# Kernel optimization log

Hardware: AMD Instinct MI355X
Metric: run time of the kernel (lower is better)

## Reference

```python
import jax, jax.numpy as jnp
import numpy as np

B, N, M, C, K = 4, 16384, 512, 256, 24
EPS = 1e-5


def setup_inputs() -> dict:
    key = jax.random.key(0)
    ks = jax.random.split(key, 5)
    return {
        "x": jax.random.normal(ks[0], (B, N, C), jnp.float32),
        "coords": jax.random.normal(ks[1], (B, N, 3), jnp.float32),
        "anchors": jax.random.normal(ks[2], (B, M, 3), jnp.float32),
        "fc_w": jax.random.normal(ks[3], (C, C), jnp.float32) * 0.05,
        "fc_b": jax.random.normal(ks[4], (C,), jnp.float32) * 0.05,
        "bn_gamma": jnp.ones((C,), jnp.float32),
        "bn_beta": jnp.zeros((C,), jnp.float32),
    }


def _build_incidence(coords, anchors):
    # squared distances suffice for top-k ordering (monotone in cdist)
    d2 = (
        jnp.sum(coords * coords, -1)[:, :, None]
        + jnp.sum(anchors * anchors, -1)[:, None, :]
        - 2.0 * jnp.einsum("bnd,bmd->bnm", coords, anchors)
    )  # [B,N,M]
    k = min(K, anchors.shape[1])
    _, idx = jax.lax.top_k(-d2, k)  # [B,N,k] nearest anchors
    b = jnp.arange(coords.shape[0])[:, None, None]
    n = jnp.arange(coords.shape[1])[None, :, None]
    H = jnp.zeros(d2.shape, d2.dtype).at[b, n, idx].set(1.0)
    return jax.lax.stop_gradient(H)  # built under torch.no_grad()


def _hypconv(x, H, fc_w, fc_b):
    xf = x @ fc_w.T + fc_b  # [B,N,C]
    deg_e = jnp.sum(H, axis=1)  # [B,M]  hyperedge degrees
    inv_e = jnp.where(deg_e > 0, 1.0 / deg_e, 0.0)[..., None]
    E = jnp.einsum("bnm,bnc->bmc", H, xf) * inv_e  # v -> e mean agg
    deg_v = jnp.sum(H, axis=2)  # [B,N]  node degrees
    inv_v = jnp.where(deg_v > 0, 1.0 / deg_v, 0.0)[..., None]
    return jnp.einsum("bnm,bmc->bnc", H, E) * inv_v  # e -> v mean agg


def reference(x, coords, anchors, fc_w, fc_b, bn_gamma, bn_beta):
    H = _build_incidence(coords, anchors)
    x = _hypconv(x, H, fc_w, fc_b) + x  # residual, [B,N,C]
    x = jnp.transpose(x, (0, 2, 1))  # [B,C,N]
    # BatchNorm1d (training-mode batch stats) over (B, N) per channel
    mean = jnp.mean(x, axis=(0, 2), keepdims=True)
    var = jnp.var(x, axis=(0, 2), keepdims=True)
    y = (x - mean) * jax.lax.rsqrt(var + EPS)
    y = y * bn_gamma[None, :, None] + bn_beta[None, :, None]
    return y * jax.nn.sigmoid(y)  # SiLU
```

## Files before the change

kernel.cpp:

```cpp
#include <hip/hip_runtime.h>

#define BB 4
#define NN 16384
#define MM 512
#define CCH 256
#define KNN 24
#define EPSV 1e-5f

typedef unsigned short ushort_t;

__device__ __forceinline__ unsigned int pk_bf16(float a, float b) {
    unsigned int ua = __float_as_uint(a), ub = __float_as_uint(b);
    ua += 0x7FFFu + ((ua >> 16) & 1u);
    ub += 0x7FFFu + ((ub >> 16) & 1u);
    return (ua >> 16) | (ub & 0xFFFF0000u);
}
__device__ __forceinline__ float lo_bf(unsigned int u) { return __uint_as_float(u << 16); }
__device__ __forceinline__ float hi_bf(unsigned int u) { return __uint_as_float(u & 0xFFFF0000u); }

__global__ __launch_bounds__(256) void k_cvt(const float* __restrict__ x,
                                             unsigned int* __restrict__ xh) {
    int i = blockIdx.x * 256 + threadIdx.x;
    float2 v = ((const float2*)x)[i];
    xh[i] = pk_bf16(v.x, v.y);
}

__global__ __launch_bounds__(256) void k_wt(const float* __restrict__ W, float* __restrict__ Wt) {
    int i = blockIdx.x * 256 + threadIdx.x;
    int co = i >> 8, ci = i & 255;
    Wt[(ci << 8) + co] = W[i];
}

#define AE(K) "v_max_u32 v89, v88, " K "\n\tv_min_u32 " K ", v88, " K "\n\t"
#define AO(K) "v_max_u32 v88, v89, " K "\n\tv_min_u32 " K ", v89, " K "\n\t"
#define BE(K) "v_max_u32 v91, v90, " K "\n\tv_min_u32 " K ", v90, " K "\n\t"
#define BO(K) "v_max_u32 v90, v91, " K "\n\tv_min_u32 " K ", v91, " K "\n\t"
#define CE(K) "v_max_u32 v93, v92, " K "\n\tv_min_u32 " K ", v92, " K "\n\t"
#define CO(K) "v_max_u32 v92, v93, " K "\n\tv_min_u32 " K ", v93, " K "\n\t"
#define DE(K) "v_max_u32 v95, v94, " K "\n\tv_min_u32 " K ", v94, " K "\n\t"
#define DO_(K) "v_max_u32 v94, v95, " K "\n\tv_min_u32 " K ", v95, " K "\n\t"
__global__ __launch_bounds__(128, 2) void k_topk(const float* __restrict__ coords,
                                                 const float* __restrict__ anchors,
                                                 ushort_t* __restrict__ idx_out,
                                                 int* __restrict__ histT) {
    __shared__ float4 alds[MM];
    __shared__ int    hist[MM];
    int tid = threadIdx.x;
    int blk = blockIdx.x;
    int b  = blk >> 8;
    int g  = blk & 255;
    int n0 = g << 6;
    int lane = tid & 63;
    int half = lane >> 5;
    int n = n0 + ((tid >> 6) << 5) + (lane & 31);

    for (int m = tid; m < MM; m += 128) {
        float x_ = anchors[(b * MM + m) * 3 + 0];
        float y_ = anchors[(b * MM + m) * 3 + 1];
        float z_ = anchors[(b * MM + m) * 3 + 2];
        alds[m] = make_float4(x_, y_, z_, x_ * x_ + y_ * y_ + z_ * z_);
        hist[m] = 0;
    }
    __syncthreads();

    float cx = coords[(b * NN + n) * 3 + 0];
    float cy = coords[(b * NN + n) * 3 + 1];
    float cz = coords[(b * NN + n) * 3 + 2];
    float cn2 = cx * cx + cy * cy + cz * cz;

    unsigned int k0 = 0xFFFFFFFFu, k1 = 0xFFFFFFFFu, k2 = 0xFFFFFFFFu, k3 = 0xFFFFFFFFu,
                 k4 = 0xFFFFFFFFu, k5 = 0xFFFFFFFFu, k6 = 0xFFFFFFFFu, k7 = 0xFFFFFFFFu,
                 k8 = 0xFFFFFFFFu, k9 = 0xFFFFFFFFu, k10 = 0xFFFFFFFFu, k11 = 0xFFFFFFFFu,
                 k12 = 0xFFFFFFFFu, k13 = 0xFFFFFFFFu, k14 = 0xFFFFFFFFu, k15 = 0xFFFFFFFFu,
                 k16 = 0xFFFFFFFFu, k17 = 0xFFFFFFFFu, k18 = 0xFFFFFFFFu, k19 = 0xFFFFFFFFu,
                 k20 = 0xFFFFFFFFu, k21 = 0xFFFFFFFFu, k22 = 0xFFFFFFFFu, k23 = 0xFFFFFFFFu;

    int base = half << 8;
    float4 a0 = alds[base + 0];
    float4 a1 = alds[base + 1];
    float4 a2 = alds[base + 2];
    float4 a3 = alds[base + 3];
    for (int mm = 0; mm < 64; ++mm) {
        int nxt = (4 * mm + 4) & 255;
        float4 p0 = alds[base + nxt + 0];
        float4 p1 = alds[base + nxt + 1];
        float4 p2 = alds[base + nxt + 2];
        float4 p3 = alds[base + nxt + 3];
        float cd0 = cn2 + a0.w - 2.0f * (cx * a0.x + cy * a0.y + cz * a0.z);
        float cd1 = cn2 + a1.w - 2.0f * (cx * a1.x + cy * a1.y + cz * a1.z);
        float cd2 = cn2 + a2.w - 2.0f * (cx * a2.x + cy * a2.y + cz * a2.z);
        float cd3 = cn2 + a3.w - 2.0f * (cx * a3.x + cy * a3.y + cz * a3.z);
        int id0 = base + 4 * mm;
        unsigned int cA = ((__float_as_uint(cd0) ^ 0x80000000u) & 0xFFFFFE00u) | (unsigned)(id0 + 0);
        unsigned int cB = ((__float_as_uint(cd1) ^ 0x80000000u) & 0xFFFFFE00u) | (unsigned)(id0 + 1);
        unsigned int cC = ((__float_as_uint(cd2) ^ 0x80000000u) & 0xFFFFFE00u) | (unsigned)(id0 + 2);
        unsigned int cD = ((__float_as_uint(cd3) ^ 0x80000000u) & 0xFFFFFE00u) | (unsigned)(id0 + 3);
        asm volatile(
            AE("v64")
            AO("v65") BE("v64")
            AE("v66") BO("v65") CE("v64")
            AO("v67") BE("v66") CO("v65") DE("v64")
            AE("v68") BO("v67") CE("v66") DO_("v65")
            AO("v69") BE("v68") CO("v67") DE("v66")
            AE("v70") BO("v69") CE("v68") DO_("v67")
            AO("v71") BE("v70") CO("v69") DE("v68")
            AE("v72") BO("v71") CE("v70") DO_("v69")
            AO("v73") BE("v72") CO("v71") DE("v70")
            AE("v74") BO("v73") CE("v72") DO_("v71")
            AO("v75") BE("v74") CO("v73") DE("v72")
            AE("v76") BO("v75") CE("v74") DO_("v73")
            AO("v77") BE("v76") CO("v75") DE("v74")
            AE("v78") BO("v77") CE("v76") DO_("v75")
            AO("v79") BE("v78") CO("v77") DE("v76")
            AE("v80") BO("v79") CE("v78") DO_("v77")
            AO("v81") BE("v80") CO("v79") DE("v78")
            AE("v82") BO("v81") CE("v80") DO_("v79")
            AO("v83") BE("v82") CO("v81") DE("v80")
            AE("v84") BO("v83") CE("v82") DO_("v81")
            AO("v85") BE("v84") CO("v83") DE("v82")
            AE("v86") BO("v85") CE("v84") DO_("v83")
            AO("v87") BE("v86") CO("v85") DE("v84")
                      BO("v87") CE("v86") DO_("v85")
                                CO("v87") DE("v86")
                                          DO_("v87")
            : "+{v64}"(k0),  "+{v65}"(k1),  "+{v66}"(k2),  "+{v67}"(k3),
              "+{v68}"(k4),  "+{v69}"(k5),  "+{v70}"(k6),  "+{v71}"(k7),
              "+{v72}"(k8),  "+{v73}"(k9),  "+{v74}"(k10), "+{v75}"(k11),
              "+{v76}"(k12), "+{v77}"(k13), "+{v78}"(k14), "+{v79}"(k15),
              "+{v80}"(k16), "+{v81}"(k17), "+{v82}"(k18), "+{v83}"(k19),
              "+{v84}"(k20), "+{v85}"(k21), "+{v86}"(k22), "+{v87}"(k23),
              "+{v88}"(cA), "+{v90}"(cB), "+{v92}"(cC), "+{v94}"(cD)
            :
            : "v89", "v91", "v93", "v95");
        a0 = p0; a1 = p1; a2 = p2; a3 = p3;
    }

    unsigned int kk[24] = {k0, k1, k2, k3, k4, k5, k6, k7, k8, k9, k10, k11,
                           k12, k13, k14, k15, k16, k17, k18, k19, k20, k21, k22, k23};

    int Mi[12];
    #pragma unroll
    for (int j = 0; j < 12; ++j) {
        unsigned int sA = __shfl_xor(kk[23 - j], 32);
        unsigned int sB = __shfl_xor(kk[12 + j], 32);
        unsigned int mi = (half == 0) ? min(kk[j], sA) : min(sB, kk[11 - j]);
        Mi[j] = (int)(mi & 511u);
    }

    #pragma unroll
    for (int j = 0; j < 12; ++j) atomicAdd(&hist[Mi[j]], 1);

    unsigned int* ob = (unsigned int*)(idx_out + (size_t)(b * NN + n) * KNN + half * 12);
    ob[0] = (unsigned)(Mi[0] | (Mi[1] << 16));
    ob[1] = (unsigned)(Mi[2] | (Mi[3] << 16));
    ob[2] = (unsigned)(Mi[4] | (Mi[5] << 16));
    ob[3] = (unsigned)(Mi[6] | (Mi[7] << 16));
    ob[4] = (unsigned)(Mi[8] | (Mi[9] << 16));
    ob[5] = (unsigned)(Mi[10] | (Mi[11] << 16));

    __syncthreads();
    for (int m = tid; m < MM; m += 128)
        histT[((((b << 9) + m)) << 8) + g] = hist[m];
}

__global__ __launch_bounds__(64) void k_scan(const int* __restrict__ histT,
                                             int* __restrict__ posT,
                                             int* __restrict__ deg) {
    int e = blockIdx.x;
    int t = threadIdx.x;
    int4 v = ((const int4*)(histT + (e << 8)))[t];
    int s = v.x + v.y + v.z + v.w;
    int inc = s;
    #pragma unroll
    for (int off = 1; off < 64; off <<= 1) {
        int u = __shfl_up(inc, off);
        if (t >= off) inc += u;
    }
    int excl = inc - s;
    int4 o;
    o.x = excl; o.y = excl + v.x; o.z = o.y + v.y; o.w = o.z + v.z;
    ((int4*)(posT + (e << 8)))[t] = o;
    if (t == 63) deg[e] = inc;
}

__global__ __launch_bounds__(256) void k_offsets(const int* __restrict__ deg,
                                                 int* __restrict__ offs) {
    __shared__ int part[256];
    int t = threadIdx.x;
    int v[8];
    int s = 0;
    #pragma unroll
    for (int j = 0; j < 8; ++j) { v[j] = deg[t * 8 + j]; s += v[j]; }
    part[t] = s;
    __syncthreads();
    for (int off = 1; off < 256; off <<= 1) {
        int val = (t >= off) ? part[t - off] : 0;
        __syncthreads();
        part[t] += val;
        __syncthreads();
    }
    int excl = part[t] - s;
    #pragma unroll
    for (int j = 0; j < 8; ++j) { offs[t * 8 + j] = excl; excl += v[j]; }
}

__global__ __launch_bounds__(256) void k_fill2(const unsigned int* __restrict__ idxu,
                                               const int* __restrict__ posT,
                                               const int* __restrict__ offs,
                                               ushort_t* __restrict__ list) {
    __shared__ int pos[MM];
    __shared__ unsigned int ebuf[768];
    int tid = threadIdx.x;
    int blk = blockIdx.x;
    int b = blk >> 8, g = blk & 255;
    int n0 = g << 6;

    for (int m = tid; m < MM; m += 256) {
        int e = (b << 9) + m;
        pos[m] = offs[e] + posT[(e << 8) + g];
    }
    for (int i = tid; i < 768; i += 256)
        ebuf[i] = idxu[(size_t)(b * NN + n0) * 12 + i];
    __syncthreads();

    for (int i = tid; i < 768; i += 256) {
        unsigned int u = ebuf[i];
        int node = n0 + (i / 12);
        int p0 = atomicAdd(&pos[u & 0xFFFFu], 1);
        list[p0] = (ushort_t)node;
        int p1 = atomicAdd(&pos[u >> 16], 1);
        list[p1] = (ushort_t)node;
    }
}

__global__ __launch_bounds__(256) void k_edge2(const unsigned int* __restrict__ xh,
                                               const ushort_t* __restrict__ list,
                                               const int* __restrict__ offs,
                                               const int* __restrict__ deg,
                                               const float* __restrict__ Wt,
                                               const float* __restrict__ fcb,
                                               unsigned int* __restrict__ Eph) {
    __shared__ ushort_t nl[256];
    __shared__ float part[2][128][2];
    __shared__ float srow[CCH];
    __shared__ float rrow[CCH];
    int tid = threadIdx.x;
    int blk = blockIdx.x;
    int b = blk >> 9;
    int d = deg[blk];
    int o = offs[blk];
    int cp = tid & 127, rs = tid >> 7;
    const unsigned int* xb = xh + ((size_t)b << 21);

    float l0 = 0.f, l1 = 0.f, l2 = 0.f, l3 = 0.f;
    float h0 = 0.f, h1 = 0.f, h2 = 0.f, h3 = 0.f;
    for (int base2 = 0; base2 < d; base2 += 256) {
        int cnt = min(256, d - base2);
        if (tid < cnt) nl[tid] = list[(size_t)o + base2 + tid];
        __syncthreads();
        int i = 0;
        for (; i + 7 < cnt; i += 8) {
            unsigned int u0 = xb[((size_t)nl[i + 0 + rs] << 7) + cp];
            unsigned int u1 = xb[((size_t)nl[i + 2 + rs] << 7) + cp];
            unsigned int u2 = xb[((size_t)nl[i + 4 + rs] << 7) + cp];
            unsigned int u3 = xb[((size_t)nl[i + 6 + rs] << 7) + cp];
            l0 += lo_bf(u0); h0 += hi_bf(u0);
            l1 += lo_bf(u1); h1 += hi_bf(u1);
            l2 += lo_bf(u2); h2 += hi_bf(u2);
            l3 += lo_bf(u3); h3 += hi_bf(u3);
        }
        for (; i + 1 < cnt; i += 2) {
            unsigned int u = xb[((size_t)nl[i + rs] << 7) + cp];
            l0 += lo_bf(u); h0 += hi_bf(u);
        }
        if (i < cnt && rs == 0) {
            unsigned int u = xb[((size_t)nl[i] << 7) + cp];
            l0 += lo_bf(u); h0 += hi_bf(u);
        }
        __syncthreads();
    }
    part[rs][cp][0] = (l0 + l1) + (l2 + l3);
    part[rs][cp][1] = (h0 + h1) + (h2 + h3);
    __syncthreads();
    float inv = (d > 0) ? (1.0f / (float)d) : 0.0f;
    srow[tid] = (part[0][tid >> 1][tid & 1] + part[1][tid >> 1][tid & 1]) * inv;
    __syncthreads();

    float c0 = (d > 0) ? fcb[tid] : 0.0f;
    float c1 = 0.f, c2 = 0.f, c3 = 0.f;
    #pragma unroll 4
    for (int ci = 0; ci < CCH; ci += 4) {
        c0 = fmaf(srow[ci + 0], Wt[((ci + 0) << 8) + tid], c0);
        c1 = fmaf(srow[ci + 1], Wt[((ci + 1) << 8) + tid], c1);
        c2 = fmaf(srow[ci + 2], Wt[((ci + 2) << 8) + tid], c2);
        c3 = fmaf(srow[ci + 3], Wt[((ci + 3) << 8) + tid], c3);
    }
    rrow[tid] = ((c0 + c1) + (c2 + c3)) * (1.0f / 24.0f);
    __syncthreads();
    if (tid < 128) Eph[(size_t)blk * 128 + tid] = pk_bf16(rrow[2 * tid], rrow[2 * tid + 1]);
}

__global__ __launch_bounds__(256) void k_gather(const float* __restrict__ x,
                                                const unsigned int* __restrict__ idxu,
                                                const unsigned int* __restrict__ Eph,
                                                float* __restrict__ out,
                                                float* __restrict__ bn1,
                                                float* __restrict__ bn2) {
    __shared__ int   it[32 * KNN];
    __shared__ float tile[32][CCH + 1];
    int tid = threadIdx.x;
    int blk = blockIdx.x;
    int b = blk >> 9;
    int n0 = (blk & 511) << 5;
    int cp = tid & 127, rs = tid >> 7;

    for (int i = tid; i < 32 * 12; i += 256) {
        unsigned int u = idxu[(size_t)(b * NN + n0) * 12 + i];
        it[2 * i] = u & 0xFFFF;
        it[2 * i + 1] = u >> 16;
    }
    __syncthreads();

    const unsigned int* Eb = Eph + ((size_t)(b * MM) << 7);
    for (int j2 = 0; j2 < 16; ++j2) {
        int j = 2 * j2 + rs;
        int n = n0 + j;
        const int* itj = &it[j * KNN];
        float al = 0.f, ah = 0.f, bl = 0.f, bh = 0.f;
        float cl = 0.f, ch = 0.f, dl = 0.f, dh = 0.f;
        #pragma unroll
        for (int k = 0; k < KNN; k += 4) {
            unsigned int u0 = Eb[((size_t)itj[k + 0] << 7) + cp];
            unsigned int u1 = Eb[((size_t)itj[k + 1] << 7) + cp];
            unsigned int u2 = Eb[((size_t)itj[k + 2] << 7) + cp];
            unsigned int u3 = Eb[((size_t)itj[k + 3] << 7) + cp];
            al += lo_bf(u0); ah += hi_bf(u0);
            bl += lo_bf(u1); bh += hi_bf(u1);
            cl += lo_bf(u2); ch += hi_bf(u2);
            dl += lo_bf(u3); dh += hi_bf(u3);
        }
        float2 xv = ((const float2*)(x + (((size_t)(b * NN + n)) << 8)))[cp];
        tile[j][2 * cp + 0] = xv.x + ((al + bl) + (cl + dl));
        tile[j][2 * cp + 1] = xv.y + ((ah + bh) + (ch + dh));
    }
    __syncthreads();

    float sum = 0.f, ss = 0.f;
    #pragma unroll 4
    for (int j = 0; j < 32; ++j) {
        float v = tile[j][tid];
        sum += v; ss += v * v;
    }
    bn1[(size_t)blk * 256 + tid] = sum;
    bn2[(size_t)blk * 256 + tid] = ss;

    for (int i = tid; i < CCH * 32; i += 256) {
        int c2 = i >> 5, j2 = i & 31;
        out[(((size_t)(b * CCH + c2)) << 14) + n0 + j2] = tile[j2][c2];
    }
}

__global__ __launch_bounds__(256) void k_stats(const float* __restrict__ bn1,
                                               const float* __restrict__ bn2,
                                               const float* __restrict__ gamma,
                                               const float* __restrict__ beta,
                                               float* __restrict__ ab) {
    __shared__ float r1[256], r2[256];
    int c = blockIdx.x;
    int t = threadIdx.x;
    float s1 = 0.f, s2 = 0.f;
    for (int i = t; i < 2048; i += 256) {
        s1 += bn1[i * 256 + c];
        s2 += bn2[i * 256 + c];
    }
    r1[t] = s1; r2[t] = s2;
    __syncthreads();
    for (int o = 128; o > 0; o >>= 1) {
        if (t < o) { r1[t] += r1[t + o]; r2[t] += r2[t + o]; }
        __syncthreads();
    }
    if (t == 0) {
        float mean = r1[0] * (1.0f / 65536.0f);
        float var  = r2[0] * (1.0f / 65536.0f) - mean * mean;
        float istd = rsqrtf(var + EPSV);
        float a = gamma[c] * istd;
        ab[c] = a;
        ab[CCH + c] = beta[c] - mean * a;
    }
}

__global__ __launch_bounds__(256) void k_silu(float* __restrict__ out,
                                              const float* __restrict__ ab) {
    int i = blockIdx.x * 256 + threadIdx.x;
    int c = (i >> 12) & 255;
    float a = ab[c], bb = ab[CCH + c];
    float4 v = ((float4*)out)[i];
    float t0 = a * v.x + bb;
    float t1 = a * v.y + bb;
    float t2 = a * v.z + bb;
    float t3 = a * v.w + bb;
    v.x = t0 / (1.0f + __expf(-t0));
    v.y = t1 / (1.0f + __expf(-t1));
    v.z = t2 / (1.0f + __expf(-t2));
    v.w = t3 / (1.0f + __expf(-t3));
    ((float4*)out)[i] = v;
}

extern "C" void kernel_launch(void* const* d_in, const int* in_sizes, int n_in,
                              void* d_out, int out_size, void* d_ws, size_t ws_size,
                              hipStream_t stream) {
    (void)in_sizes; (void)n_in; (void)out_size; (void)ws_size;
    const float* x       = (const float*)d_in[0];
    const float* coords  = (const float*)d_in[1];
    const float* anchors = (const float*)d_in[2];
    const float* fcw     = (const float*)d_in[3];
    const float* fcb     = (const float*)d_in[4];
    const float* gamma   = (const float*)d_in[5];
    const float* beta    = (const float*)d_in[6];
    float* out = (float*)d_out;

    unsigned int* xh = (unsigned int*)d_out;

    char* ws = (char*)d_ws;
    ushort_t*     ws_idx   = (ushort_t*)    (ws + 0);
    int*          ws_deg   = (int*)         (ws + 3145728);
    int*          ws_offs  = (int*)         (ws + 3153920);
    ushort_t*     ws_list  = (ushort_t*)    (ws + 3162112);
    int*          ws_histT = (int*)         (ws + 6307840);
    int*          ws_posT  = (int*)         (ws + 8404992);
    unsigned int* ws_eph   = (unsigned int*)(ws + 10502144);
    float*        ws_wt    = (float*)       (ws + 11550720);
    float*        ws_bn1   = (float*)       (ws + 11812864);
    float*        ws_bn2   = (float*)       (ws + 13910016);
    float*        ws_ab    = (float*)       (ws + 16007168);

    hipLaunchKernelGGL(k_cvt,     dim3(32768), dim3(256), 0, stream, x, xh);
    hipLaunchKernelGGL(k_wt,      dim3(256),   dim3(256), 0, stream, fcw, ws_wt);
    hipLaunchKernelGGL(k_topk,    dim3(1024),  dim3(128), 0, stream, coords, anchors, ws_idx, ws_histT);
    hipLaunchKernelGGL(k_scan,    dim3(2048),  dim3(64),  0, stream, ws_histT, ws_posT, ws_deg);
    hipLaunchKernelGGL(k_offsets, dim3(1),     dim3(256), 0, stream, ws_deg, ws_offs);
    hipLaunchKernelGGL(k_fill2,   dim3(1024),  dim3(256), 0, stream, (const unsigned int*)ws_idx, ws_posT, ws_offs, ws_list);
    hipLaunchKernelGGL(k_edge2,   dim3(2048),  dim3(256), 0, stream, xh, ws_list, ws_offs, ws_deg, ws_wt, fcb, ws_eph);
    hipLaunchKernelGGL(k_gather,  dim3(2048),  dim3(256), 0, stream, x, (const unsigned int*)ws_idx, ws_eph, out, ws_bn1, ws_bn2);
    hipLaunchKernelGGL(k_stats,   dim3(256),   dim3(256), 0, stream, ws_bn1, ws_bn2, gamma, beta, ws_ab);
    hipLaunchKernelGGL(k_silu,    dim3(16384), dim3(256), 0, stream, out, ws_ab);
}
```

Measured before the change: 293.2 us.

## Split hyperedge aggregation across channel quarters and separate the FC matvec

The per-hyperedge sum over member nodes now runs as 8192 blocks, each covering one quarter of the channels with 8 row-slices in flight, and writes fp32 partial sums to a new workspace buffer. A separate kernel then applies the mean, the FC weight matvec and the bias, and packs the result to bf16. The aim is more parallelism and better load balance for the gather-heavy edge aggregation, which is sensitive to uneven hyperedge degrees. In exchange it adds an extra launch and a round trip of the partial sums through global memory, and each block reads only 128-byte row segments.

```diff
diff --git a/kernel.cpp b/kernel.cpp
--- a/kernel.cpp
+++ b/kernel.cpp
@@ -233,57 +233,70 @@
     }
 }
 
-__global__ __launch_bounds__(256) void k_edge2(const unsigned int* __restrict__ xh,
-                                               const ushort_t* __restrict__ list,
-                                               const int* __restrict__ offs,
-                                               const int* __restrict__ deg,
-                                               const float* __restrict__ Wt,
-                                               const float* __restrict__ fcb,
-                                               unsigned int* __restrict__ Eph) {
+__global__ __launch_bounds__(256) void k_edge2a(const unsigned int* __restrict__ xh,
+                                                const ushort_t* __restrict__ list,
+                                                const int* __restrict__ offs,
+                                                const int* __restrict__ deg,
+                                                float* __restrict__ S) {
     __shared__ ushort_t nl[256];
-    __shared__ float part[2][128][2];
-    __shared__ float srow[CCH];
-    __shared__ float rrow[CCH];
+    __shared__ float red[8][64];
     int tid = threadIdx.x;
-    int blk = blockIdx.x;
-    int b = blk >> 9;
-    int d = deg[blk];
-    int o = offs[blk];
-    int cp = tid & 127, rs = tid >> 7;
-    const unsigned int* xb = xh + ((size_t)b << 21);
-
-    float l0 = 0.f, l1 = 0.f, l2 = 0.f, l3 = 0.f;
-    float h0 = 0.f, h1 = 0.f, h2 = 0.f, h3 = 0.f;
+    int bi = blockIdx.x;
+    int r = bi >> 12;
+    int grp = (bi & 7) | (r << 3);
+    int b = grp & 3;
+    int q = grp >> 2;
+    int e = (b << 9) | ((bi >> 3) & 511);
+    int d = deg[e];
+    int o = offs[e];
+    int cp = tid & 31, rs = tid >> 5;
+    const unsigned int* xb = xh + ((size_t)b << 21) + (q << 5);
+
+    float l0 = 0.f, h0 = 0.f, l1 = 0.f, h1 = 0.f;
     for (int base2 = 0; base2 < d; base2 += 256) {
         int cnt = min(256, d - base2);
         if (tid < cnt) nl[tid] = list[(size_t)o + base2 + tid];
         __syncthreads();
         int i = 0;
-        for (; i + 7 < cnt; i += 8) {
-            unsigned int u0 = xb[((size_t)nl[i + 0 + rs] << 7) + cp];
-            unsigned int u1 = xb[((size_t)nl[i + 2 + rs] << 7) + cp];
-            unsigned int u2 = xb[((size_t)nl[i + 4 + rs] << 7) + cp];
-            unsigned int u3 = xb[((size_t)nl[i + 6 + rs] << 7) + cp];
+        for (; i + 15 < cnt; i += 16) {
+            unsigned int u0 = xb[((size_t)nl[i + rs] << 7) + cp];
+            unsigned int u1 = xb[((size_t)nl[i + 8 + rs] << 7) + cp];
             l0 += lo_bf(u0); h0 += hi_bf(u0);
             l1 += lo_bf(u1); h1 += hi_bf(u1);
-            l2 += lo_bf(u2); h2 += hi_bf(u2);
-            l3 += lo_bf(u3); h3 += hi_bf(u3);
         }
-        for (; i + 1 < cnt; i += 2) {
+        for (; i + 7 < cnt; i += 8) {
             unsigned int u = xb[((size_t)nl[i + rs] << 7) + cp];
             l0 += lo_bf(u); h0 += hi_bf(u);
         }
-        if (i < cnt && rs == 0) {
-            unsigned int u = xb[((size_t)nl[i] << 7) + cp];
-            l0 += lo_bf(u); h0 += hi_bf(u);
+        if (i + rs < cnt) {
+            unsigned int u = xb[((size_t)nl[i + rs] << 7) + cp];
+            l1 += lo_bf(u); h1 += hi_bf(u);
         }
         __syncthreads();
     }
-    part[rs][cp][0] = (l0 + l1) + (l2 + l3);
-    part[rs][cp][1] = (h0 + h1) + (h2 + h3);
-    __syncthreads();
+    red[rs][2 * cp] = l0 + l1;
+    red[rs][2 * cp + 1] = h0 + h1;
+    __syncthreads();
+    if (tid < 64) {
+        float s = 0.f;
+        #pragma unroll
+        for (int j = 0; j < 8; ++j) s += red[j][tid];
+        S[((size_t)e << 8) + (q << 6) + tid] = s;
+    }
+}
+
+__global__ __launch_bounds__(256) void k_edge2b(const float* __restrict__ S,
+                                                const int* __restrict__ deg,
+                                                const float* __restrict__ Wt,
+                                                const float* __restrict__ fcb,
+                                                unsigned int* __restrict__ Eph) {
+    __shared__ float srow[CCH];
+    __shared__ float rrow[CCH];
+    int tid = threadIdx.x;
+    int e = blockIdx.x;
+    int d = deg[e];
     float inv = (d > 0) ? (1.0f / (float)d) : 0.0f;
-    srow[tid] = (part[0][tid >> 1][tid & 1] + part[1][tid >> 1][tid & 1]) * inv;
+    srow[tid] = S[((size_t)e << 8) + tid] * inv;
     __syncthreads();
 
     float c0 = (d > 0) ? fcb[tid] : 0.0f;
@@ -297,7 +310,7 @@
     }
     rrow[tid] = ((c0 + c1) + (c2 + c3)) * (1.0f / 24.0f);
     __syncthreads();
-    if (tid < 128) Eph[(size_t)blk * 128 + tid] = pk_bf16(rrow[2 * tid], rrow[2 * tid + 1]);
+    if (tid < 128) Eph[((size_t)e << 7) + tid] = pk_bf16(rrow[2 * tid], rrow[2 * tid + 1]);
 }
 
 __global__ __launch_bounds__(256) void k_gather(const float* __restrict__ x,
@@ -429,10 +442,11 @@
     int*          ws_histT = (int*)         (ws + 6307840);
     int*          ws_posT  = (int*)         (ws + 8404992);
     unsigned int* ws_eph   = (unsigned int*)(ws + 10502144);
-    float*        ws_wt    = (float*)       (ws + 11550720);
-    float*        ws_bn1   = (float*)       (ws + 11812864);
-    float*        ws_bn2   = (float*)       (ws + 13910016);
-    float*        ws_ab    = (float*)       (ws + 16007168);
+    float*        ws_S     = (float*)       (ws + 11550720);
+    float*        ws_wt    = (float*)       (ws + 13647872);
+    float*        ws_bn1   = (float*)       (ws + 13910016);
+    float*        ws_bn2   = (float*)       (ws + 16007168);
+    float*        ws_ab    = (float*)       (ws + 18104320);
 
     hipLaunchKernelGGL(k_cvt,     dim3(32768), dim3(256), 0, stream, x, xh);
     hipLaunchKernelGGL(k_wt,      dim3(256),   dim3(256), 0, stream, fcw, ws_wt);
@@ -440,7 +454,8 @@
     hipLaunchKernelGGL(k_scan,    dim3(2048),  dim3(64),  0, stream, ws_histT, ws_posT, ws_deg);
     hipLaunchKernelGGL(k_offsets, dim3(1),     dim3(256), 0, stream, ws_deg, ws_offs);
     hipLaunchKernelGGL(k_fill2,   dim3(1024),  dim3(256), 0, stream, (const unsigned int*)ws_idx, ws_posT, ws_offs, ws_list);
-    hipLaunchKernelGGL(k_edge2,   dim3(2048),  dim3(256), 0, stream, xh, ws_list, ws_offs, ws_deg, ws_wt, fcb, ws_eph);
+    hipLaunchKernelGGL(k_edge2a,  dim3(8192),  dim3(256), 0, stream, xh, ws_list, ws_offs, ws_deg, ws_S);
+    hipLaunchKernelGGL(k_edge2b,  dim3(2048),  dim3(256), 0, stream, ws_S, ws_deg, ws_wt, fcb, ws_eph);
     hipLaunchKernelGGL(k_gather,  dim3(2048),  dim3(256), 0, stream, x, (const unsigned int*)ws_idx, ws_eph, out, ws_bn1, ws_bn2);
     hipLaunchKernelGGL(k_stats,   dim3(256),   dim3(256), 0, stream, ws_bn1, ws_bn2, gamma, beta, ws_ab);
     hipLaunchKernelGGL(k_silu,    dim3(16384), dim3(256), 0, stream, out, ws_ab);
```

New measurement: 294.2 us. Within noise of the previous version (+0.3%).
